# Kernel tuning notes

Hardware: AMD Instinct MI355X
Metric: run time of the kernel (lower is better)

## Reference

```python
import jax, jax.numpy as jnp
import numpy as np


def setup_inputs() -> dict:
    key = jax.random.key(0)
    k1, k2 = jax.random.split(key)
    B, D, L = 32, 64, 4096
    N_CB, K = 4, 512
    x_in = jax.random.normal(k1, (B, D, L), dtype=jnp.float32)
    # torch.rand(num_tokens, token_dim) per codebook -> uniform [0,1)
    codebooks = jax.random.uniform(k2, (N_CB, K, D), dtype=jnp.float32)
    return {"x_in": x_in, "codebooks": codebooks}


def _vq_select(x_res, emb):
    """Nearest-code quantization for one codebook.

    x_res: [B, D, L], emb: [K, D]
    Returns z_q [B, D, L], idx [B, L].
    """
    x_t = jnp.transpose(x_res, (0, 2, 1))  # [B, L, D]
    # squared euclidean distances via GEMM (same argmin as torch.cdist)
    d2 = (
        jnp.sum(x_t * x_t, axis=-1, keepdims=True)
        - 2.0 * jnp.einsum("bld,kd->blk", x_t, emb)
        + jnp.sum(emb * emb, axis=-1)
    )  # [B, L, K]
    idx = jnp.argmin(d2, axis=-1)  # [B, L]
    z_q = jnp.transpose(emb[idx], (0, 2, 1))  # [B, D, L]
    return z_q, idx


def reference(x_in, codebooks):
    """Residual VQ: per codebook quantize the residual, accumulate sums.

    Returns z_q_aggregated [B, n_cb, D, L] (cumulative sums) and
    indices [B, L, n_cb].
    """
    n_cb = codebooks.shape[0]
    x_res = x_in
    z_q = jnp.zeros_like(x_in)
    agg = []
    idx_list = []
    for c in range(n_cb):  # small fixed loop over codebooks
        z_q_ind, idx = _vq_select(x_res, codebooks[c])
        x_res = x_res - z_q_ind
        z_q = z_q + z_q_ind
        agg.append(z_q)
        idx_list.append(idx)
    z_q_aggregated = jnp.stack(agg, axis=1)  # [B, n_cb, D, L]
    indices = jnp.stack(idx_list, axis=-1)  # [B, L, n_cb]
    return z_q_aggregated, indices
```

## Files before the change

### kernel.cpp

```cpp
#include <hip/hip_runtime.h>


#define LL   4096
#define DD   64
#define KK   512
#define NCB  4
#define TB   32
#define NTHR 256
#define XS   36
#define ES   260
#define EBUFN (16 * ES)

#define ZQ_ELEMS (32LL * NCB * DD * LL)

__device__ __forceinline__ float np_pairwise_sq64(const float* p) {
#pragma clang fp contract(off)
    float r[8];
#pragma unroll
    for (int j = 0; j < 8; ++j) { float s = p[j] * p[j]; r[j] = s; }
#pragma unroll
    for (int i = 8; i < 64; i += 8)
#pragma unroll
        for (int j = 0; j < 8; ++j) { float s = p[i + j] * p[i + j]; r[j] = r[j] + s; }
    return ((r[0] + r[1]) + (r[2] + r[3])) + ((r[4] + r[5]) + (r[6] + r[7]));
}

__global__ void se_kernel(const float* __restrict__ cb, float* __restrict__ se) {
    int t = blockIdx.x * blockDim.x + threadIdx.x;
    if (t >= NCB * KK) return;
    se[t] = np_pairwise_sq64(cb + (size_t)t * DD);
}

__global__ __launch_bounds__(NTHR) void rvq_kernel(const float* __restrict__ x_in,
                                                   const float* __restrict__ cb,
                                                   const float* __restrict__ se,
                                                   float* __restrict__ out) {
    __shared__ float ebuf[2 * EBUFN];
    __shared__ float x_lds[DD * XS];

    const int tid  = threadIdx.x;
    const int lane = tid & 63;
    const int w8   = (tid >> 6) << 3;

    const long T0 = (long)blockIdx.x * TB;
    const int b  = (int)(T0 >> 12);
    const int l0 = (int)(T0 & 4095);

    {
        const float* xb = x_in + (size_t)b * DD * LL + l0;
        const int dd0 = tid >> 3;
        const int t4  = (tid & 7) << 2;
#pragma unroll
        for (int it = 0; it < 2; ++it) {
            const int d = it * 32 + dd0;
            const float4 v = *reinterpret_cast<const float4*>(xb + (size_t)d * LL + t4);
            *reinterpret_cast<float4*>(&x_lds[d * XS + t4]) = v;
        }
    }

    const int sq = tid & 3;
    const int sk = tid >> 2;

    float4 sv0, sv1, sv2, sv3;
    {
        const float* ec = cb + (size_t)(sq << 2);
        sv0 = *reinterpret_cast<const float4*>(ec + (size_t)(sk +   0) * DD);
        sv1 = *reinterpret_cast<const float4*>(ec + (size_t)(sk +  64) * DD);
        sv2 = *reinterpret_cast<const float4*>(ec + (size_t)(sk + 128) * DD);
        sv3 = *reinterpret_cast<const float4*>(ec + (size_t)(sk + 192) * DD);
    }

    __syncthreads();

    float zq[8];
#pragma unroll
    for (int t = 0; t < 8; ++t) zq[t] = 0.f;

    const int sxj = lane & 7;
    const int sxt = lane >> 3;
    const int myt = lane & 7;
    const int da  = lane >> 3;

#pragma unroll 1
    for (int c = 0; c < NCB; ++c) {
        float a3;
        {
            float r;
            {
#pragma clang fp contract(off)
                float p = x_lds[sxj * XS + w8 + sxt];
                r = p * p;
#pragma unroll
                for (int i = 1; i < 8; ++i) {
                    float q = x_lds[(i * 8 + sxj) * XS + w8 + sxt];
                    r = r + q * q;
                }
            }
            float o1 = __shfl_xor(r, 1, 64);
            float a1 = r + o1;
            float o2 = __shfl_xor(a1, 2, 64);
            float a2 = a1 + o2;
            float o4 = __shfl_xor(a2, 4, 64);
            a3 = a2 + o4;
        }

        float b1v[8]; int b1i[8];
#pragma unroll
        for (int t = 0; t < 8; ++t) { b1v[t] = __builtin_inff(); b1i[t] = 0; }

        float acc[8][4];

#pragma unroll 1
        for (int s = 0; s < 8; ++s) {
            float* eb = &ebuf[(s & 1) * EBUFN];

            eb[(sq * 4 + 0) * ES + sk      ] = sv0.x;
            eb[(sq * 4 + 1) * ES + sk      ] = sv0.y;
            eb[(sq * 4 + 2) * ES + sk      ] = sv0.z;
            eb[(sq * 4 + 3) * ES + sk      ] = sv0.w;
            eb[(sq * 4 + 0) * ES + sk +  64] = sv1.x;
            eb[(sq * 4 + 1) * ES + sk +  64] = sv1.y;
            eb[(sq * 4 + 2) * ES + sk +  64] = sv1.z;
            eb[(sq * 4 + 3) * ES + sk +  64] = sv1.w;
            eb[(sq * 4 + 0) * ES + sk + 128] = sv2.x;
            eb[(sq * 4 + 1) * ES + sk + 128] = sv2.y;
            eb[(sq * 4 + 2) * ES + sk + 128] = sv2.z;
            eb[(sq * 4 + 3) * ES + sk + 128] = sv2.w;
            eb[(sq * 4 + 0) * ES + sk + 192] = sv3.x;
            eb[(sq * 4 + 1) * ES + sk + 192] = sv3.y;
            eb[(sq * 4 + 2) * ES + sk + 192] = sv3.z;
            eb[(sq * 4 + 3) * ES + sk + 192] = sv3.w;

            __syncthreads();

            {
                int nc = c, ns = s + 1;
                if (ns == 8) { nc = c + 1; ns = 0; }
                if (nc < NCB) {
                    const float* ec = cb + ((size_t)(nc * KK + (ns >> 2) * 256)) * DD
                                         + (size_t)((ns & 3) * 16 + (sq << 2));
                    sv0 = *reinterpret_cast<const float4*>(ec + (size_t)(sk +   0) * DD);
                    sv1 = *reinterpret_cast<const float4*>(ec + (size_t)(sk +  64) * DD);
                    sv2 = *reinterpret_cast<const float4*>(ec + (size_t)(sk + 128) * DD);
                    sv3 = *reinterpret_cast<const float4*>(ec + (size_t)(sk + 192) * DD);
                }
            }

            if ((s & 3) == 0) {
#pragma unroll
                for (int t = 0; t < 8; ++t)
#pragma unroll
                    for (int g = 0; g < 4; ++g) acc[t][g] = 0.f;
            }

            const int mbase = (s & 3) * 16;
#pragma unroll
            for (int dd = 0; dd < 16; ++dd) {
                const int d = mbase + dd;
                const float4 e4  = *reinterpret_cast<const float4*>(&eb[dd * ES + (lane << 2)]);
                const float4 xa  = *reinterpret_cast<const float4*>(&x_lds[d * XS + w8]);
                const float4 xb4 = *reinterpret_cast<const float4*>(&x_lds[d * XS + w8 + 4]);
                const float xv[8] = {xa.x, xa.y, xa.z, xa.w, xb4.x, xb4.y, xb4.z, xb4.w};
                const float ev[4] = {e4.x, e4.y, e4.z, e4.w};
#pragma unroll
                for (int t = 0; t < 8; ++t)
#pragma unroll
                    for (int g = 0; g < 4; ++g)
                        acc[t][g] = fmaf(xv[t], ev[g], acc[t][g]);
            }

            if ((s & 3) == 3) {
#pragma clang fp contract(off)
                const int kb = (s >> 2) * 256 + (lane << 2);
                const float4 se4 = *reinterpret_cast<const float4*>(&se[c * KK + kb]);
                const float sev[4] = {se4.x, se4.y, se4.z, se4.w};
#pragma unroll
                for (int t = 0; t < 8; ++t) {
                    const float sxv = __shfl(a3, t << 3, 64);
#pragma unroll
                    for (int g = 0; g < 4; ++g) {
                        const float twod = 2.0f * acc[t][g];
                        const float d2 = (sxv - twod) + sev[g];
                        if (d2 < b1v[t]) { b1v[t] = d2; b1i[t] = kb + g; }
                    }
                }
            }
        }

#pragma unroll
        for (int t = 0; t < 8; ++t) {
            float v = b1v[t]; int i = b1i[t];
#pragma unroll
            for (int off = 32; off > 0; off >>= 1) {
                const float ov = __shfl_xor(v, off, 64);
                const int   oi = __shfl_xor(i, off, 64);
                if (ov < v || (ov == v && oi < i)) { v = ov; i = oi; }
            }
            b1i[t] = i;
        }

        int kown = 0;
#pragma unroll
        for (int t = 0; t < 8; ++t) if (myt == t) kown = b1i[t];

        {
#pragma clang fp contract(off)
            const float* erow = cb + ((size_t)(c * KK) + kown) * DD + da;
#pragma unroll
            for (int i = 0; i < 8; ++i) {
                const float ev = erow[i * 8];
                const int xi = (i * 8 + da) * XS + w8 + myt;
                x_lds[xi] = x_lds[xi] - ev;
                zq[i] = zq[i] + ev;
            }
        }

#pragma unroll
        for (int t = 0; t < 8; ++t)
            if (lane == t)
                out[ZQ_ELEMS + ((size_t)b * LL + l0 + w8 + t) * NCB + c] = (float)b1i[t];

#pragma unroll
        for (int i = 0; i < 8; ++i)
            ebuf[(i * 8 + da) * XS + w8 + myt] = zq[i];
        __syncthreads();
        {
            float* zo = out + (((size_t)b * NCB + c) * DD) * LL + l0;
            const int c4 = (tid & 7) << 2;
            const int d0 = tid >> 3;
#pragma unroll
            for (int p = 0; p < 2; ++p) {
                const int d = p * 32 + d0;
                const float4 v = *reinterpret_cast<const float4*>(&ebuf[d * XS + c4]);
                *reinterpret_cast<float4*>(zo + (size_t)d * LL + c4) = v;
            }
        }
        __syncthreads();
    }
}

extern "C" void kernel_launch(void* const* d_in, const int* in_sizes, int n_in,
                              void* d_out, int out_size, void* d_ws, size_t ws_size,
                              hipStream_t stream) {
    const float* x_in = (const float*)d_in[0];
    const float* cb   = (const float*)d_in[1];
    float* out = (float*)d_out;
    float* se  = (float*)d_ws;

    se_kernel<<<dim3((NCB * KK + 255) / 256), dim3(256), 0, stream>>>(cb, se);
    rvq_kernel<<<dim3((32 * LL) / TB), dim3(NTHR), 0, stream>>>(x_in, cb, se, out);
}
```

Baseline: 631.4 us.

## Double token tile per block to 64 with 16 tokens per wave

Each block now processes 64 tokens instead of 32, and each wave computes a 16-token by 4-code register tile instead of 8 by 4. Every codebook value staged in LDS is therefore reused across twice as many tokens, which halves the codebook staging traffic and barriers per token. The cost is higher register pressure (64 accumulators plus 16 best values and indices), half as many blocks, and a larger x tile in LDS, all of which may lower occupancy.

```diff
diff --git a/kernel.cpp b/kernel.cpp
--- a/kernel.cpp
+++ b/kernel.cpp
@@ -5,10 +5,11 @@
 #define DD   64
 #define KK   512
 #define NCB  4
-#define TB   32
+#define TB   64
 #define NTHR 256
-#define XS   36
+#define XS   72
 #define ES   260
+#define EZ   64
 #define EBUFN (16 * ES)
 
 #define ZQ_ELEMS (32LL * NCB * DD * LL)
@@ -40,7 +41,7 @@
 
     const int tid  = threadIdx.x;
     const int lane = tid & 63;
-    const int w8   = (tid >> 6) << 3;
+    const int w16  = (tid >> 6) << 4;
 
     const long T0 = (long)blockIdx.x * TB;
     const int b  = (int)(T0 >> 12);
@@ -48,13 +49,12 @@
 
     {
         const float* xb = x_in + (size_t)b * DD * LL + l0;
-        const int dd0 = tid >> 3;
-        const int t4  = (tid & 7) << 2;
-#pragma unroll
-        for (int it = 0; it < 2; ++it) {
-            const int d = it * 32 + dd0;
-            const float4 v = *reinterpret_cast<const float4*>(xb + (size_t)d * LL + t4);
-            *reinterpret_cast<float4*>(&x_lds[d * XS + t4]) = v;
+#pragma unroll
+        for (int it = 0; it < 4; ++it) {
+            const int d = (tid >> 4) + it * 16;
+            const int q = (tid & 15) << 2;
+            const float4 v = *reinterpret_cast<const float4*>(xb + (size_t)d * LL + q);
+            *reinterpret_cast<float4*>(&x_lds[d * XS + q]) = v;
         }
     }
 
@@ -72,43 +72,56 @@
 
     __syncthreads();
 
-    float zq[8];
-#pragma unroll
-    for (int t = 0; t < 8; ++t) zq[t] = 0.f;
+    float zq[16];
+#pragma unroll
+    for (int t = 0; t < 16; ++t) zq[t] = 0.f;
 
     const int sxj = lane & 7;
     const int sxt = lane >> 3;
-    const int myt = lane & 7;
-    const int da  = lane >> 3;
+    const int myt = lane & 15;
+    const int da  = lane >> 4;
 
 #pragma unroll 1
     for (int c = 0; c < NCB; ++c) {
-        float a3;
+        float a3lo, a3hi;
         {
             float r;
             {
 #pragma clang fp contract(off)
-                float p = x_lds[sxj * XS + w8 + sxt];
+                float p = x_lds[sxj * XS + w16 + sxt];
                 r = p * p;
 #pragma unroll
                 for (int i = 1; i < 8; ++i) {
-                    float q = x_lds[(i * 8 + sxj) * XS + w8 + sxt];
+                    float q = x_lds[(i * 8 + sxj) * XS + w16 + sxt];
                     r = r + q * q;
                 }
             }
-            float o1 = __shfl_xor(r, 1, 64);
-            float a1 = r + o1;
-            float o2 = __shfl_xor(a1, 2, 64);
-            float a2 = a1 + o2;
-            float o4 = __shfl_xor(a2, 4, 64);
-            a3 = a2 + o4;
-        }
-
-        float b1v[8]; int b1i[8];
-#pragma unroll
-        for (int t = 0; t < 8; ++t) { b1v[t] = __builtin_inff(); b1i[t] = 0; }
-
-        float acc[8][4];
+            float o1 = __shfl_xor(r, 1, 64);  float a1 = r + o1;
+            float o2 = __shfl_xor(a1, 2, 64); float a2 = a1 + o2;
+            float o4 = __shfl_xor(a2, 4, 64); a3lo = a2 + o4;
+        }
+        {
+            float r;
+            {
+#pragma clang fp contract(off)
+                float p = x_lds[sxj * XS + w16 + 8 + sxt];
+                r = p * p;
+#pragma unroll
+                for (int i = 1; i < 8; ++i) {
+                    float q = x_lds[(i * 8 + sxj) * XS + w16 + 8 + sxt];
+                    r = r + q * q;
+                }
+            }
+            float o1 = __shfl_xor(r, 1, 64);  float a1 = r + o1;
+            float o2 = __shfl_xor(a1, 2, 64); float a2 = a1 + o2;
+            float o4 = __shfl_xor(a2, 4, 64); a3hi = a2 + o4;
+        }
+
+        float b1v[16]; int b1i[16];
+#pragma unroll
+        for (int t = 0; t < 16; ++t) { b1v[t] = __builtin_inff(); b1i[t] = 0; }
+
+        float acc[16][4];
 
 #pragma unroll 1
         for (int s = 0; s < 8; ++s) {
@@ -148,7 +161,7 @@
 
             if ((s & 3) == 0) {
 #pragma unroll
-                for (int t = 0; t < 8; ++t)
+                for (int t = 0; t < 16; ++t)
 #pragma unroll
                     for (int g = 0; g < 4; ++g) acc[t][g] = 0.f;
             }
@@ -157,16 +170,21 @@
 #pragma unroll
             for (int dd = 0; dd < 16; ++dd) {
                 const int d = mbase + dd;
-                const float4 e4  = *reinterpret_cast<const float4*>(&eb[dd * ES + (lane << 2)]);
-                const float4 xa  = *reinterpret_cast<const float4*>(&x_lds[d * XS + w8]);
-                const float4 xb4 = *reinterpret_cast<const float4*>(&x_lds[d * XS + w8 + 4]);
-                const float xv[8] = {xa.x, xa.y, xa.z, xa.w, xb4.x, xb4.y, xb4.z, xb4.w};
-                const float ev[4] = {e4.x, e4.y, e4.z, e4.w};
-#pragma unroll
-                for (int t = 0; t < 8; ++t)
-#pragma unroll
-                    for (int g = 0; g < 4; ++g)
-                        acc[t][g] = fmaf(xv[t], ev[g], acc[t][g]);
+                const float4 e4 = *reinterpret_cast<const float4*>(&eb[dd * ES + (lane << 2)]);
+                const float4 x0 = *reinterpret_cast<const float4*>(&x_lds[d * XS + w16]);
+                const float4 x1 = *reinterpret_cast<const float4*>(&x_lds[d * XS + w16 + 4]);
+                const float4 x2 = *reinterpret_cast<const float4*>(&x_lds[d * XS + w16 + 8]);
+                const float4 x3 = *reinterpret_cast<const float4*>(&x_lds[d * XS + w16 + 12]);
+#define FMA4(T, XV)                                   \
+                acc[T][0] = fmaf(XV, e4.x, acc[T][0]); \
+                acc[T][1] = fmaf(XV, e4.y, acc[T][1]); \
+                acc[T][2] = fmaf(XV, e4.z, acc[T][2]); \
+                acc[T][3] = fmaf(XV, e4.w, acc[T][3]);
+                FMA4( 0, x0.x) FMA4( 1, x0.y) FMA4( 2, x0.z) FMA4( 3, x0.w)
+                FMA4( 4, x1.x) FMA4( 5, x1.y) FMA4( 6, x1.z) FMA4( 7, x1.w)
+                FMA4( 8, x2.x) FMA4( 9, x2.y) FMA4(10, x2.z) FMA4(11, x2.w)
+                FMA4(12, x3.x) FMA4(13, x3.y) FMA4(14, x3.z) FMA4(15, x3.w)
+#undef FMA4
             }
 
             if ((s & 3) == 3) {
@@ -175,8 +193,8 @@
                 const float4 se4 = *reinterpret_cast<const float4*>(&se[c * KK + kb]);
                 const float sev[4] = {se4.x, se4.y, se4.z, se4.w};
 #pragma unroll
-                for (int t = 0; t < 8; ++t) {
-                    const float sxv = __shfl(a3, t << 3, 64);
+                for (int t = 0; t < 16; ++t) {
+                    const float sxv = __shfl((t < 8) ? a3lo : a3hi, (t & 7) << 3, 64);
 #pragma unroll
                     for (int g = 0; g < 4; ++g) {
                         const float twod = 2.0f * acc[t][g];
@@ -188,7 +206,7 @@
         }
 
 #pragma unroll
-        for (int t = 0; t < 8; ++t) {
+        for (int t = 0; t < 16; ++t) {
             float v = b1v[t]; int i = b1i[t];
 #pragma unroll
             for (int off = 32; off > 0; off >>= 1) {
@@ -201,38 +219,37 @@
 
         int kown = 0;
 #pragma unroll
-        for (int t = 0; t < 8; ++t) if (myt == t) kown = b1i[t];
+        for (int t = 0; t < 16; ++t) if (myt == t) kown = b1i[t];
 
         {
 #pragma clang fp contract(off)
             const float* erow = cb + ((size_t)(c * KK) + kown) * DD + da;
 #pragma unroll
-            for (int i = 0; i < 8; ++i) {
-                const float ev = erow[i * 8];
-                const int xi = (i * 8 + da) * XS + w8 + myt;
+            for (int i = 0; i < 16; ++i) {
+                const float ev = erow[i * 4];
+                const int xi = (i * 4 + da) * XS + w16 + myt;
                 x_lds[xi] = x_lds[xi] - ev;
                 zq[i] = zq[i] + ev;
             }
         }
 
 #pragma unroll
-        for (int t = 0; t < 8; ++t)
+        for (int t = 0; t < 16; ++t)
             if (lane == t)
-                out[ZQ_ELEMS + ((size_t)b * LL + l0 + w8 + t) * NCB + c] = (float)b1i[t];
-
-#pragma unroll
-        for (int i = 0; i < 8; ++i)
-            ebuf[(i * 8 + da) * XS + w8 + myt] = zq[i];
+                out[ZQ_ELEMS + ((size_t)b * LL + l0 + w16 + t) * NCB + c] = (float)b1i[t];
+
+#pragma unroll
+        for (int i = 0; i < 16; ++i)
+            ebuf[(i * 4 + da) * EZ + w16 + myt] = zq[i];
         __syncthreads();
         {
             float* zo = out + (((size_t)b * NCB + c) * DD) * LL + l0;
-            const int c4 = (tid & 7) << 2;
-            const int d0 = tid >> 3;
-#pragma unroll
-            for (int p = 0; p < 2; ++p) {
-                const int d = p * 32 + d0;
-                const float4 v = *reinterpret_cast<const float4*>(&ebuf[d * XS + c4]);
-                *reinterpret_cast<float4*>(zo + (size_t)d * LL + c4) = v;
+#pragma unroll
+            for (int it = 0; it < 4; ++it) {
+                const int d = (tid >> 4) + it * 16;
+                const int q = (tid & 15) << 2;
+                const float4 v = *reinterpret_cast<const float4*>(&ebuf[d * EZ + q]);
+                *reinterpret_cast<float4*>(zo + (size_t)d * LL + q) = v;
             }
         }
         __syncthreads();
```

New measurement: 964.6 us. +52.8%, slower.
